# Kernel optimization log

Hardware: AMD Instinct MI355X
Metric: run time of the kernel (lower is better)

Reference implementation:

```python
import jax, jax.numpy as jnp
import numpy as np
import math

N_HEAD = 16
DEG = 2
EPS = 1e-7


def setup_inputs() -> dict:
    key = jax.random.key(0)
    k1, k2 = jax.random.split(key)
    B, T, C = 2, 2048, 1024
    x = jax.random.normal(k1, (B, T, C), dtype=jnp.float32)
    W = jax.random.normal(k2, (3 * C + N_HEAD, C), dtype=jnp.float32) * (1.0 / math.sqrt(C))
    return {"x": x, "W": W}


def reference(x, W):
    # JacobAttentionLayer.forward with attention_kernel='powerref' (AttentionReference,
    # deg=2, scale=1/sqrt(hs), eps=1e-7, log-space power softmax, gating=True).
    B, T, C = x.shape
    nh = N_HEAD
    hs = C // nh
    scale = 1.0 / math.sqrt(hs)

    qkvgr = jnp.einsum('btc,oc->bto', x, W)  # [B,T,3C+nh]
    q, k, v = (qkvgr[..., :C], qkvgr[..., C:2 * C], qkvgr[..., 2 * C:3 * C])
    log_g = jax.nn.log_sigmoid(qkvgr[..., 3 * C:].astype(jnp.float32))  # [B,T,nh]
    log_G = jnp.cumsum(log_g, axis=1).transpose(0, 2, 1)  # [B,nh,T]

    def heads(a):  # [B,T,C] -> [B,nh,T,hs]
        return a.reshape(B, T, nh, hs).transpose(0, 2, 1, 3)

    Q, K, V = heads(q), heads(k), heads(v)

    S = jnp.einsum('bhtd,bhsd->bhts', Q, K)  # [B,nh,T,T]
    # log-space power attention: deg*log(|S|+eps) + log(scale) + gating
    Tm = DEG * jnp.log(jnp.abs(S) + EPS) + jnp.log(jnp.float32(scale))
    Z = Tm + log_G[..., :, None] - log_G[..., None, :]
    mask = jnp.tril(jnp.ones((T, T), dtype=bool))
    Z = jnp.where(mask, Z, -jnp.inf)
    Z_rowmax = jax.lax.stop_gradient(jnp.max(Z, axis=-1, keepdims=True))
    P = jnp.exp(Z - Z_rowmax)  # deg even -> no sign correction

    norm = jnp.sum(P, axis=-1)  # [B,nh,T]
    O = jnp.einsum('bhts,bhsd->bhtd', P, V)
    y = O / norm[..., None]
    return y.transpose(0, 2, 1, 3).reshape(B, T, C)
```

## Files before the change

kernel.cpp:

```cpp
#include <hip/hip_runtime.h>
#include <math.h>

typedef __attribute__((ext_vector_type(4))) float f32x4;
typedef __attribute__((ext_vector_type(8))) short short8;

#define NEG_INF (-__builtin_inff())

__device__ __forceinline__ unsigned short f2bf(float f) {
    union { float f; unsigned u; } v; v.f = f;
    unsigned r = v.u + 0x7FFFu + ((v.u >> 16) & 1u);
    return (unsigned short)(r >> 16);
}
__device__ __forceinline__ float bf2f(unsigned short h) {
    union { unsigned u; float f; } v; v.u = ((unsigned)h) << 16;
    return v.f;
}

__device__ __forceinline__ f32x4 mfma_bf16(short8 a, short8 b, f32x4 c) {
    return __builtin_amdgcn_mfma_f32_16x16x32_bf16(a, b, c, 0, 0, 0);
}

__device__ __forceinline__ void gload_lds16(const unsigned short* g, unsigned short* l) {
    __builtin_amdgcn_global_load_lds(
        (const __attribute__((address_space(1))) void*)g,
        (__attribute__((address_space(3))) void*)l, 16, 0, 0);
}

__global__ void split_kernel(const float* __restrict__ in,
                             unsigned short* __restrict__ hi,
                             unsigned short* __restrict__ lo, int n4)
{
    int i = blockIdx.x * 256 + threadIdx.x;
    if (i >= n4) return;
    float4 v = ((const float4*)in)[i];
    ushort4 h, l;
    h.x = f2bf(v.x); l.x = f2bf(v.x - bf2f(h.x));
    h.y = f2bf(v.y); l.y = f2bf(v.y - bf2f(h.y));
    h.z = f2bf(v.z); l.z = f2bf(v.z - bf2f(h.z));
    h.w = f2bf(v.w); l.w = f2bf(v.w - bf2f(h.w));
    ((ushort4*)hi)[i] = h;
    ((ushort4*)lo)[i] = l;
}

__global__ __launch_bounds__(256, 2)
void gemm_proj(const unsigned short* __restrict__ xh, const unsigned short* __restrict__ xl,
               const unsigned short* __restrict__ wh, const unsigned short* __restrict__ wl,
               unsigned short* __restrict__ Qh, unsigned short* __restrict__ Ql,
               unsigned short* __restrict__ Kh, unsigned short* __restrict__ Kl,
               unsigned short* __restrict__ Vtg, float* __restrict__ gbuf)
{
    __shared__ __align__(16) unsigned short Ah[2][128][32];
    __shared__ __align__(16) unsigned short Al[2][128][32];
    __shared__ __align__(16) unsigned short Bh[2][128][32];
    __shared__ __align__(16) unsigned short Bl[2][128][32];

    const int mt = blockIdx.x & 31;
    const int nt = blockIdx.x >> 5;
    const int m0 = mt * 128, n0 = nt * 128;
    const int tid = threadIdx.x;
    const int w = tid >> 6, l = tid & 63;
    const int wm = w >> 1, wn = w & 1;
    const int lr = l & 15, lq = l >> 4;
    const int xs = (lr >> 1) & 3;
    const bool needLo = (nt < 16) || (nt == 24);

    f32x4 acc[4][4];
#pragma unroll
    for (int i = 0; i < 4; ++i)
#pragma unroll
        for (int j = 0; j < 4; ++j) acc[i][j] = (f32x4){0.f, 0.f, 0.f, 0.f};

    const int srow = tid >> 2;
    const int sp = tid & 3;

    auto STAGE = [&](int bsel, int k0) {
#pragma unroll
        for (int p = 0; p < 2; ++p) {
            int r = srow + p * 64;
            int sc = (sp ^ ((r >> 1) & 3)) * 8;
            int o = n0 + r;
            int oc = o < 3088 ? o : 3087;
            gload_lds16(&xh[(size_t)(m0 + r) * 1024 + k0 + sc], &Ah[bsel][r][sp * 8]);
            gload_lds16(&wh[(size_t)oc * 1024 + k0 + sc],       &Bh[bsel][r][sp * 8]);
            if (needLo) {
                gload_lds16(&xl[(size_t)(m0 + r) * 1024 + k0 + sc], &Al[bsel][r][sp * 8]);
                gload_lds16(&wl[(size_t)oc * 1024 + k0 + sc],       &Bl[bsel][r][sp * 8]);
            }
        }
    };

    STAGE(0, 0);
    __asm__ volatile("s_waitcnt vmcnt(0)" ::: "memory");
    __syncthreads();

    int cur = 0;
    for (int k0 = 0; k0 < 1024; k0 += 32) {
        if (k0 + 32 < 1024) STAGE(cur ^ 1, k0 + 32);

        short8 ah[4], bh4[4], al4[4], bl4[4];
#pragma unroll
        for (int i = 0; i < 4; ++i) {
            ah[i]  = *(const short8*)&Ah[cur][wm * 64 + i * 16 + lr][(lq ^ xs) * 8];
            bh4[i] = *(const short8*)&Bh[cur][wn * 64 + i * 16 + lr][(lq ^ xs) * 8];
        }
        if (needLo) {
#pragma unroll
            for (int i = 0; i < 4; ++i) {
                al4[i] = *(const short8*)&Al[cur][wm * 64 + i * 16 + lr][(lq ^ xs) * 8];
                bl4[i] = *(const short8*)&Bl[cur][wn * 64 + i * 16 + lr][(lq ^ xs) * 8];
            }
        }
#pragma unroll
        for (int i = 0; i < 4; ++i)
#pragma unroll
            for (int j = 0; j < 4; ++j) {
                acc[i][j] = mfma_bf16(ah[i], bh4[j], acc[i][j]);
                if (needLo) {
                    acc[i][j] = mfma_bf16(ah[i], bl4[j], acc[i][j]);
                    acc[i][j] = mfma_bf16(al4[i], bh4[j], acc[i][j]);
                }
            }

        __asm__ volatile("s_waitcnt vmcnt(0)" ::: "memory");
        __syncthreads();
        cur ^= 1;
    }

#pragma unroll
    for (int i = 0; i < 4; ++i) {
        int nrow0 = m0 + wm * 64 + i * 16 + lq * 4;
        int b = nrow0 >> 11;
        int tbase = nrow0 & 2047;
#pragma unroll
        for (int j = 0; j < 4; ++j) {
            int o = n0 + wn * 64 + j * 16 + lr;
            if (o < 1024) {
                int h = o >> 6, d = o & 63;
                size_t base = ((size_t)(b * 16 + h) * 2048 + tbase) * 64 + d;
#pragma unroll
                for (int r = 0; r < 4; ++r) {
                    float v = acc[i][j][r];
                    unsigned short hi_ = f2bf(v);
                    unsigned short lo_ = f2bf(v - bf2f(hi_));
                    Qh[base + (size_t)r * 64] = hi_;
                    Ql[base + (size_t)r * 64] = lo_;
                }
            } else if (o < 2048) {
                int oo = o - 1024;
                int h = oo >> 6, d = oo & 63;
                size_t base = ((size_t)(b * 16 + h) * 2048 + tbase) * 64 + d;
#pragma unroll
                for (int r = 0; r < 4; ++r) {
                    float v = acc[i][j][r];
                    unsigned short hi_ = f2bf(v);
                    unsigned short lo_ = f2bf(v - bf2f(hi_));
                    Kh[base + (size_t)r * 64] = hi_;
                    Kl[base + (size_t)r * 64] = lo_;
                }
            } else if (o < 3072) {
                int oo = o - 2048;
                int h = oo >> 6, d = oo & 63;
                size_t base = ((size_t)(b * 16 + h) * 64 + d) * 2048 + tbase;
                ushort4 pk;
                pk.x = f2bf(acc[i][j][0]);
                pk.y = f2bf(acc[i][j][1]);
                pk.z = f2bf(acc[i][j][2]);
                pk.w = f2bf(acc[i][j][3]);
                *(ushort4*)&Vtg[base] = pk;
            } else if (o < 3088) {
                int og = o - 3072;
#pragma unroll
                for (int r = 0; r < 4; ++r)
                    gbuf[(size_t)(nrow0 + r) * 16 + og] = acc[i][j][r];
            }
        }
    }
}

__global__ void gate_scan(const float* __restrict__ g, float* __restrict__ lg)
{
    const int bh = blockIdx.x;
    const int b = bh >> 4, h = bh & 15;
    const int tid = threadIdx.x;
    __shared__ float part[256];

    float vals[8];
    float run = 0.f;
#pragma unroll
    for (int j = 0; j < 8; ++j) {
        int t = tid * 8 + j;
        float x = g[(size_t)(b * 2048 + t) * 16 + h];
        float ls = fminf(x, 0.f) - log1pf(__expf(-fabsf(x)));
        run += ls * 1.4426950408889634f;
        vals[j] = run;
    }
    part[tid] = run;
    __syncthreads();
    for (int ofs = 1; ofs < 256; ofs <<= 1) {
        float add = (tid >= ofs) ? part[tid - ofs] : 0.f;
        __syncthreads();
        part[tid] += add;
        __syncthreads();
    }
    float excl = part[tid] - run;
#pragma unroll
    for (int j = 0; j < 8; ++j)
        lg[(size_t)bh * 2048 + tid * 8 + j] = excl + vals[j];
}

__global__ __launch_bounds__(256, 3)
void attn_fwd(const unsigned short* __restrict__ Qh, const unsigned short* __restrict__ Ql,
              const unsigned short* __restrict__ Kh, const unsigned short* __restrict__ Kl,
              const unsigned short* __restrict__ Vtg, const float* __restrict__ lg,
              float* __restrict__ out)
{
    __shared__ __align__(16) unsigned short kh[2][64][64];
    __shared__ __align__(16) unsigned short kl[2][64][64];
    __shared__ __align__(16) unsigned short pl[4][16][64];

    const int bid = blockIdx.x;
    const int x8 = bid & 7;
    const int k  = bid >> 3;
    const int m  = k >> 2;
    const int bh = x8 + 8 * (k & 3);
    const int qi = (m & 1) ? (31 - (m >> 1)) : (m >> 1);
    const int tid = threadIdx.x;
    const int w = tid >> 6, l = tid & 63;
    const int lr = l & 15, lq = l >> 4;
    const int xk = lr & 7;
    const int q0 = qi * 64;
    const int myrow0 = q0 + w * 16;

    const size_t qoff = ((size_t)bh * 2048 + myrow0 + lr) * 64;
    short8 qh8[2], ql8[2];
    qh8[0] = *(const short8*)&Qh[qoff + lq * 8];
    qh8[1] = *(const short8*)&Qh[qoff + 32 + lq * 8];
    ql8[0] = *(const short8*)&Ql[qoff + lq * 8];
    ql8[1] = *(const short8*)&Ql[qoff + 32 + lq * 8];

    float gq2[4];
#pragma unroll
    for (int r = 0; r < 4; ++r)
        gq2[r] = lg[(size_t)bh * 2048 + myrow0 + lq * 4 + r] - 3.0f;

    float M_[4]  = {0.f, 0.f, 0.f, 0.f};
    float ls_[4] = {0.f, 0.f, 0.f, 0.f};
    f32x4 o4[4];
#pragma unroll
    for (int i = 0; i < 4; ++i) o4[i] = (f32x4){0.f, 0.f, 0.f, 0.f};

    const int srow = tid >> 3;
    const int schunk = tid & 7;

    const unsigned short* Kh_b = Kh + (size_t)bh * 2048 * 64;
    const unsigned short* Kl_b = Kl + (size_t)bh * 2048 * 64;
    const unsigned short* Vt_b = Vtg + (size_t)bh * 64 * 2048;

    auto STAGE = [&](int bsel, int kv0) {
#pragma unroll
        for (int p = 0; p < 2; ++p) {
            int r = srow + p * 32;
            int sc = (schunk ^ (r & 7)) * 8;
            gload_lds16(&Kh_b[(size_t)(kv0 + r) * 64 + sc], &kh[bsel][r][schunk * 8]);
            gload_lds16(&Kl_b[(size_t)(kv0 + r) * 64 + sc], &kl[bsel][r][schunk * 8]);
        }
    };

    STAGE(0, 0);
    __asm__ volatile("s_waitcnt vmcnt(0)" ::: "memory");
    __syncthreads();

    int cur = 0;
    for (int kv0 = 0; kv0 <= q0; kv0 += 64) {
        uint4 vreg[8];
#pragma unroll
        for (int ds_ = 0; ds_ < 4; ++ds_) {
            const unsigned short* vp = &Vt_b[(size_t)(ds_ * 16 + lr) * 2048 + kv0 + lq * 8];
            vreg[ds_ * 2]     = *(const uint4*)vp;
            vreg[ds_ * 2 + 1] = *(const uint4*)(vp + 32);
        }
        if (kv0 + 64 <= q0) STAGE(cur ^ 1, kv0 + 64);

        float gsl[4];
#pragma unroll
        for (int js = 0; js < 4; ++js)
            gsl[js] = lg[(size_t)bh * 2048 + kv0 + js * 16 + lr];

        f32x4 sa[4];
#pragma unroll
        for (int js = 0; js < 4; ++js) sa[js] = (f32x4){0.f, 0.f, 0.f, 0.f};
#pragma unroll
        for (int js = 0; js < 4; ++js)
#pragma unroll
            for (int ks = 0; ks < 2; ++ks) {
                short8 kb  = *(const short8*)&kh[cur][js * 16 + lr][((ks * 4 + lq) ^ xk) << 3];
                short8 kbl = *(const short8*)&kl[cur][js * 16 + lr][((ks * 4 + lq) ^ xk) << 3];
                sa[js] = mfma_bf16(qh8[ks], kb,  sa[js]);
                sa[js] = mfma_bf16(qh8[ks], kbl, sa[js]);
                sa[js] = mfma_bf16(ql8[ks], kb,  sa[js]);
            }

        const bool diag = (kv0 == q0);
#pragma unroll
        for (int js = 0; js < 4; ++js) {
            float ga = gsl[js];
#pragma unroll
            for (int r = 0; r < 4; ++r) {
                float a = fabsf(sa[js][r]) + 1e-7f;
                float ex = exp2f(gq2[r] - ga);
                float wv = a * a * ex;
                if (diag && (js * 16 + lr > w * 16 + lq * 4 + r)) wv = 0.f;
                sa[js][r] = wv;
            }
        }

        float f_[4], rMv[4];
#pragma unroll
        for (int r = 0; r < 4; ++r) {
            float a = fmaxf(fmaxf(sa[0][r], sa[1][r]), fmaxf(sa[2][r], sa[3][r]));
#pragma unroll
            for (int msk = 1; msk < 16; msk <<= 1)
                a = fmaxf(a, __shfl_xor(a, msk, 16));
            float Mn = fmaxf(M_[r], a);
            bool pos = Mn > 1e-30f;
            float rM = pos ? __builtin_amdgcn_rcpf(Mn) : 0.f;
            f_[r]  = pos ? M_[r] * rM : 1.f;
            rMv[r] = rM;
            M_[r]  = Mn;
        }

        float rs_[4] = {0.f, 0.f, 0.f, 0.f};
#pragma unroll
        for (int js = 0; js < 4; ++js)
#pragma unroll
            for (int r = 0; r < 4; ++r) {
                float pv = sa[js][r] * rMv[r];
                sa[js][r] = pv;
                rs_[r] += pv;
            }
#pragma unroll
        for (int r = 0; r < 4; ++r) {
            float s = rs_[r];
#pragma unroll
            for (int msk = 1; msk < 16; msk <<= 1)
                s += __shfl_xor(s, msk, 16);
            ls_[r] = ls_[r] * f_[r] + s;
        }
#pragma unroll
        for (int ds_ = 0; ds_ < 4; ++ds_)
#pragma unroll
            for (int r = 0; r < 4; ++r)
                o4[ds_][r] *= f_[r];

#pragma unroll
        for (int js = 0; js < 4; ++js)
#pragma unroll
            for (int r = 0; r < 4; ++r) {
                int prow = lq * 4 + r;
                int cch = (js * 2 + (lr >> 3)) ^ (prow & 7);
                pl[w][prow][(cch << 3) | (lr & 7)] = f2bf(sa[js][r]);
            }
        __asm__ volatile("s_waitcnt lgkmcnt(0)" ::: "memory");
        __builtin_amdgcn_sched_barrier(0);

        short8 pa0 = *(const short8*)&pl[w][lr][((0 + lq) ^ xk) << 3];
        short8 pa1 = *(const short8*)&pl[w][lr][((4 + lq) ^ xk) << 3];
#pragma unroll
        for (int ds_ = 0; ds_ < 4; ++ds_) {
            short8 vb0 = *(const short8*)&vreg[ds_ * 2];
            short8 vb1 = *(const short8*)&vreg[ds_ * 2 + 1];
            o4[ds_] = mfma_bf16(pa0, vb0, o4[ds_]);
            o4[ds_] = mfma_bf16(pa1, vb1, o4[ds_]);
        }

        __asm__ volatile("s_waitcnt vmcnt(0)" ::: "memory");
        __syncthreads();
        cur ^= 1;
    }

    const int b = bh >> 4, h = bh & 15;
#pragma unroll
    for (int ds_ = 0; ds_ < 4; ++ds_)
#pragma unroll
        for (int r = 0; r < 4; ++r) {
            int t = myrow0 + lq * 4 + r;
            out[(size_t)(b * 2048 + t) * 1024 + h * 64 + ds_ * 16 + lr] =
                o4[ds_][r] / ls_[r];
        }
}

extern "C" void kernel_launch(void* const* d_in, const int* in_sizes, int n_in,
                              void* d_out, int out_size, void* d_ws, size_t ws_size,
                              hipStream_t stream)
{
    const float* x = (const float*)d_in[0];
    const float* W = (const float*)d_in[1];
    float* out = (float*)d_out;

    const size_t NX = 4194304;
    const size_t NW = 3162112;
    const size_t NQ = 4194304;

    char* ws = (char*)d_ws;
    size_t off = 0;
    auto alloc = [&](size_t bytes) -> void* {
        void* p = ws + off;
        off += (bytes + 255) & ~(size_t)255;
        return p;
    };
    unsigned short* xh = (unsigned short*)alloc(NX * 2);
    unsigned short* xl = (unsigned short*)alloc(NX * 2);
    unsigned short* wh = (unsigned short*)alloc(NW * 2);
    unsigned short* wl = (unsigned short*)alloc(NW * 2);
    unsigned short* Qh = (unsigned short*)alloc(NQ * 2);
    unsigned short* Ql = (unsigned short*)alloc(NQ * 2);
    unsigned short* Kh = (unsigned short*)alloc(NQ * 2);
    unsigned short* Kl = (unsigned short*)alloc(NQ * 2);
    unsigned short* Vt = (unsigned short*)alloc(NQ * 2);
    float* g  = (float*)alloc(65536 * 4);
    float* lg = (float*)alloc(65536 * 4);
    if (off > ws_size) return;

    split_kernel<<<(int)(NX / 4 + 255) / 256, 256, 0, stream>>>(x, xh, xl, (int)(NX / 4));
    split_kernel<<<(int)(NW / 4 + 255) / 256, 256, 0, stream>>>(W, wh, wl, (int)(NW / 4));
    gemm_proj<<<800, 256, 0, stream>>>(xh, xl, wh, wl, Qh, Ql, Kh, Kl, Vt, g);
    gate_scan<<<32, 256, 0, stream>>>(g, lg);
    attn_fwd<<<1024, 256, 0, stream>>>(Qh, Ql, Kh, Kl, Vt, lg, out);
}
```

Before: 204.0 us.

## Drop online max rescaling and compute row sums via MFMA with ones

Removes the per-tile running row maximum, its shuffle reductions, reciprocal and rescaling of the output accumulators, relying on gated weights staying in a safe float range. The row normaliser is now accumulated by two extra MFMAs of the bf16 P tile against a ones vector. P is converted to bf16 by truncation instead of round-to-nearest. This cuts VALU and cross-lane work per tile, at the risk of overflow or precision loss if unnormalised weights get large and of slightly biased truncation.

New measurement: 200.0 us. Within noise of the previous version (-2.0%).

```diff
diff --git a/kernel.cpp b/kernel.cpp
--- a/kernel.cpp
+++ b/kernel.cpp
@@ -10,6 +10,10 @@
     union { float f; unsigned u; } v; v.f = f;
     unsigned r = v.u + 0x7FFFu + ((v.u >> 16) & 1u);
     return (unsigned short)(r >> 16);
+}
+__device__ __forceinline__ unsigned short f2bf_trunc(float f) {
+    union { float f; unsigned u; } v; v.f = f;
+    return (unsigned short)(v.u >> 16);
 }
 __device__ __forceinline__ float bf2f(unsigned short h) {
     union { unsigned u; float f; } v; v.u = ((unsigned)h) << 16;
@@ -243,11 +247,14 @@
     for (int r = 0; r < 4; ++r)
         gq2[r] = lg[(size_t)bh * 2048 + myrow0 + lq * 4 + r] - 3.0f;
 
-    float M_[4]  = {0.f, 0.f, 0.f, 0.f};
-    float ls_[4] = {0.f, 0.f, 0.f, 0.f};
+    f32x4 ls4 = (f32x4){0.f, 0.f, 0.f, 0.f};
     f32x4 o4[4];
 #pragma unroll
     for (int i = 0; i < 4; ++i) o4[i] = (f32x4){0.f, 0.f, 0.f, 0.f};
+
+    short8 ones8;
+#pragma unroll
+    for (int j = 0; j < 8; ++j) ones8[j] = (short)0x3F80;
 
     const int srow = tid >> 3;
     const int schunk = tid & 7;
@@ -314,57 +321,22 @@
             }
         }
 
-        float f_[4], rMv[4];
-#pragma unroll
-        for (int r = 0; r < 4; ++r) {
-            float a = fmaxf(fmaxf(sa[0][r], sa[1][r]), fmaxf(sa[2][r], sa[3][r]));
-#pragma unroll
-            for (int msk = 1; msk < 16; msk <<= 1)
-                a = fmaxf(a, __shfl_xor(a, msk, 16));
-            float Mn = fmaxf(M_[r], a);
-            bool pos = Mn > 1e-30f;
-            float rM = pos ? __builtin_amdgcn_rcpf(Mn) : 0.f;
-            f_[r]  = pos ? M_[r] * rM : 1.f;
-            rMv[r] = rM;
-            M_[r]  = Mn;
-        }
-
-        float rs_[4] = {0.f, 0.f, 0.f, 0.f};
-#pragma unroll
-        for (int js = 0; js < 4; ++js)
-#pragma unroll
-            for (int r = 0; r < 4; ++r) {
-                float pv = sa[js][r] * rMv[r];
-                sa[js][r] = pv;
-                rs_[r] += pv;
-            }
-#pragma unroll
-        for (int r = 0; r < 4; ++r) {
-            float s = rs_[r];
-#pragma unroll
-            for (int msk = 1; msk < 16; msk <<= 1)
-                s += __shfl_xor(s, msk, 16);
-            ls_[r] = ls_[r] * f_[r] + s;
-        }
-#pragma unroll
-        for (int ds_ = 0; ds_ < 4; ++ds_)
-#pragma unroll
-            for (int r = 0; r < 4; ++r)
-                o4[ds_][r] *= f_[r];
-
 #pragma unroll
         for (int js = 0; js < 4; ++js)
 #pragma unroll
             for (int r = 0; r < 4; ++r) {
                 int prow = lq * 4 + r;
                 int cch = (js * 2 + (lr >> 3)) ^ (prow & 7);
-                pl[w][prow][(cch << 3) | (lr & 7)] = f2bf(sa[js][r]);
+                pl[w][prow][(cch << 3) | (lr & 7)] = f2bf_trunc(sa[js][r]);
             }
         __asm__ volatile("s_waitcnt lgkmcnt(0)" ::: "memory");
         __builtin_amdgcn_sched_barrier(0);
 
         short8 pa0 = *(const short8*)&pl[w][lr][((0 + lq) ^ xk) << 3];
         short8 pa1 = *(const short8*)&pl[w][lr][((4 + lq) ^ xk) << 3];
+
+        ls4 = mfma_bf16(pa0, ones8, ls4);
+        ls4 = mfma_bf16(pa1, ones8, ls4);
 #pragma unroll
         for (int ds_ = 0; ds_ < 4; ++ds_) {
             short8 vb0 = *(const short8*)&vreg[ds_ * 2];
@@ -385,7 +357,7 @@
         for (int r = 0; r < 4; ++r) {
             int t = myrow0 + lq * 4 + r;
             out[(size_t)(b * 2048 + t) * 1024 + h * 64 + ds_ * 16 + lr] =
-                o4[ds_][r] / ls_[r];
+                o4[ds_][r] / ls4[r];
         }
 }
 
```
